# Performance work log

Measured on AMD Instinct MI355X. Metric: run time of the kernel, lower is better.

The kernel has to match this reference:

```python
import jax, jax.numpy as jnp
import numpy as np

ALPHA = 0.2  # LeakyReLU negative slope


def setup_inputs() -> dict:
    key = jax.random.key(0)
    k1, k2, k3, k4 = jax.random.split(key, 4)
    N, IN, OUT = 8192, 512, 256
    x = jax.random.normal(k1, (N, IN), dtype=jnp.float32)
    adj = jnp.zeros((N, N), dtype=jnp.float32)  # accepted but unused by the module
    W = jax.random.normal(k2, (OUT, IN), dtype=jnp.float32) * (1.0 / np.sqrt(IN))
    a1 = jax.random.normal(k3, (OUT,), dtype=jnp.float32) * (1.0 / np.sqrt(OUT))
    a2 = jax.random.normal(k4, (OUT,), dtype=jnp.float32) * (1.0 / np.sqrt(OUT))
    return {"x": x, "adj": adj, "W": W, "a1": a1, "a2": a2}


def reference(x, adj, W, a1, a2):
    # h = tran(x): [N, OUT]
    h = x @ W.T
    # additive GAT scores: e[i, j] = a2 . h_i + a1 . h_j  (from unsqueeze(0)+unsqueeze(1))
    s1 = h @ a1  # [N], att1(h)
    s2 = h @ a2  # [N], att2(h)
    e = s2[:, None] + s1[None, :]  # [N, N]
    e = jnp.where(e > 0, e, ALPHA * e)  # LeakyReLU
    attn = jax.nn.softmax(e, axis=1)  # softmax over dim=1; dropout is identity in eval
    return attn @ h  # [N, OUT]
```

## Files before the change

kernel.cpp:

```cpp
#include <hip/hip_runtime.h>

#define NROW 8192
#define DIN  512
#define DOUT 256
#define NCHUNK 256
#define CLEN 32
#define JCH 8

constexpr size_t OFF_H      = 0;
constexpr size_t OFF_S1     = OFF_H + (size_t)NROW*DOUT*4;
constexpr size_t OFF_S2     = OFF_S1 + NROW*4;
constexpr size_t OFF_S1S    = OFF_S2 + NROW*4;
constexpr size_t OFF_PERM   = OFF_S1S + NROW*4;
constexpr size_t OFF_WHI    = OFF_PERM + NROW*4;
constexpr size_t OFF_WLO    = OFF_WHI + NROW*4;
constexpr size_t OFF_PRELOS = OFF_WLO + NROW*4;
constexpr size_t OFF_SUFHIS = OFF_PRELOS + 33024;
constexpr size_t OFF_MISC   = OFF_SUFHIS + 33024;
constexpr size_t OFF_PC     = OFF_MISC + 256;
constexpr size_t OFF_TLO    = OFF_PC + (size_t)JCH*NROW*4;
constexpr size_t OFF_THI    = OFF_TLO + (size_t)NCHUNK*DOUT*4;
constexpr size_t OFF_PRELO  = OFF_THI + (size_t)NCHUNK*DOUT*4;
constexpr size_t OFF_SUFHI  = OFF_PRELO + (size_t)(NROW+1)*DOUT*4;
constexpr size_t WS_NEED    = OFF_SUFHI + (size_t)(NROW+1)*DOUT*4;

__global__ __launch_bounds__(256) void gemm_h(const float* __restrict__ x,
                                              const float* __restrict__ W,
                                              const float* __restrict__ a1,
                                              const float* __restrict__ a2,
                                              float* __restrict__ h,
                                              float* __restrict__ s1,
                                              float* __restrict__ s2) {
  __shared__ float xs[64][68];
  __shared__ float ws[64][68];
  const int tid = threadIdx.x;
  const int rowBase = blockIdx.x * 64;
  const int colBase = blockIdx.y * 64;
  const int ty = tid >> 4, tx = tid & 15;
  float acc[4][4] = {};
  for (int k0 = 0; k0 < DIN; k0 += 64) {
#pragma unroll
    for (int i = 0; i < 4; ++i) {
      int s = i * 256 + tid;
      int r = s >> 4;
      int kk = (s & 15) << 2;
      float4 v = *(const float4*)(x + (size_t)(rowBase + r) * DIN + k0 + kk);
      xs[kk + 0][r] = v.x; xs[kk + 1][r] = v.y; xs[kk + 2][r] = v.z; xs[kk + 3][r] = v.w;
      float4 u = *(const float4*)(W + (size_t)(colBase + r) * DIN + k0 + kk);
      ws[kk + 0][r] = u.x; ws[kk + 1][r] = u.y; ws[kk + 2][r] = u.z; ws[kk + 3][r] = u.w;
    }
    __syncthreads();
#pragma unroll
    for (int kk = 0; kk < 64; ++kk) {
      float4 av = *(const float4*)&xs[kk][ty << 2];
      float4 bv = *(const float4*)&ws[kk][tx << 2];
      float a[4] = {av.x, av.y, av.z, av.w};
      float b[4] = {bv.x, bv.y, bv.z, bv.w};
#pragma unroll
      for (int r = 0; r < 4; ++r)
#pragma unroll
        for (int c = 0; c < 4; ++c) acc[r][c] = fmaf(a[r], b[c], acc[r][c]);
    }
    __syncthreads();
  }
#pragma unroll
  for (int r = 0; r < 4; ++r) {
    float4 o = make_float4(acc[r][0], acc[r][1], acc[r][2], acc[r][3]);
    *(float4*)(h + (size_t)(rowBase + (ty << 2) + r) * DOUT + colBase + (tx << 2)) = o;
  }
  float4 A1 = *(const float4*)(a1 + colBase + (tx << 2));
  float4 A2 = *(const float4*)(a2 + colBase + (tx << 2));
#pragma unroll
  for (int r = 0; r < 4; ++r) {
    float p1 = acc[r][0] * A1.x + acc[r][1] * A1.y + acc[r][2] * A1.z + acc[r][3] * A1.w;
    float p2 = acc[r][0] * A2.x + acc[r][1] * A2.y + acc[r][2] * A2.z + acc[r][3] * A2.w;
#pragma unroll
    for (int m = 1; m < 16; m <<= 1) {
      p1 += __shfl_xor(p1, m);
      p2 += __shfl_xor(p2, m);
    }
    if (tx == 0) {
      int row = rowBase + (ty << 2) + r;
      atomicAdd(&s1[row], p1);
      atomicAdd(&s2[row], p2);
    }
  }
}

__global__ __launch_bounds__(256) void rank_partial(const float* __restrict__ s1,
                                                    int* __restrict__ pc) {
  __shared__ float sj[1024];
  const int t = threadIdx.x;
  const int ib = blockIdx.x, jc = blockIdx.y;
  const int j0 = jc * 1024;
  *(float4*)&sj[t << 2] = *(const float4*)(s1 + j0 + (t << 2));
  const int i = ib * 256 + t;
  const float v = s1[i];
  __syncthreads();
  int cnt = 0;
#pragma unroll 4
  for (int q = 0; q < 256; ++q) {
    float4 sv = *(const float4*)&sj[q << 2];
    int jg = j0 + (q << 2);
    cnt += (int)(sv.x < v) + (int)((sv.x == v) & (jg + 0 < i));
    cnt += (int)(sv.y < v) + (int)((sv.y == v) & (jg + 1 < i));
    cnt += (int)(sv.z < v) + (int)((sv.z == v) & (jg + 2 < i));
    cnt += (int)(sv.w < v) + (int)((sv.w == v) & (jg + 3 < i));
  }
  pc[jc * NROW + i] = cnt;
}

__global__ __launch_bounds__(256) void scatter_rank(const float* __restrict__ s1,
                                                    const int* __restrict__ pc,
                                                    float* __restrict__ s1s,
                                                    int* __restrict__ perm) {
  const int i = blockIdx.x * 256 + threadIdx.x;
  int r = 0;
#pragma unroll
  for (int jc = 0; jc < JCH; ++jc) r += pc[jc * NROW + i];
  s1s[r] = s1[i];
  perm[r] = i;
}

__global__ __launch_bounds__(1024) void scan_exp(const float* __restrict__ s1s,
                                                 float* __restrict__ w_hi,
                                                 float* __restrict__ w_lo,
                                                 float* __restrict__ prelo_s,
                                                 float* __restrict__ sufhi_s,
                                                 float* __restrict__ misc) {
  __shared__ float tt[1024];
  const int t = threadIdx.x;
  const float M1 = s1s[NROW - 1];
  float kv[8];
  {
    float4 r1 = *(const float4*)(s1s + 8 * t);
    float4 r2 = *(const float4*)(s1s + 8 * t + 4);
    kv[0] = r1.x; kv[1] = r1.y; kv[2] = r1.z; kv[3] = r1.w;
    kv[4] = r2.x; kv[5] = r2.y; kv[6] = r2.z; kv[7] = r2.w;
  }

  float wl[8];
  float loc = 0.f;
#pragma unroll
  for (int e = 0; e < 8; ++e) { wl[e] = __expf(0.2f * (kv[e] - M1)); loc += wl[e]; }
  tt[t] = loc;
  __syncthreads();
  for (int off = 1; off < 1024; off <<= 1) {
    float v = (t >= off) ? tt[t - off] : 0.f;
    __syncthreads();
    tt[t] += v;
    __syncthreads();
  }
  float run = (t > 0) ? tt[t - 1] : 0.f;
#pragma unroll
  for (int e = 0; e < 8; ++e) {
    int j = 8 * t + e;
    prelo_s[j] = run;
    w_lo[j] = wl[e];
    run += wl[e];
  }
  if (t == 1023) prelo_s[NROW] = run;
  __syncthreads();

  float wh[8];
  loc = 0.f;
#pragma unroll
  for (int e = 0; e < 8; ++e) { wh[e] = __expf(kv[e] - M1); loc += wh[e]; }
  tt[t] = loc;
  __syncthreads();
  for (int off = 1; off < 1024; off <<= 1) {
    float v = (t >= off) ? tt[t - off] : 0.f;
    __syncthreads();
    tt[t] += v;
    __syncthreads();
  }
  float total = tt[1023];
  run = (t > 0) ? tt[t - 1] : 0.f;
#pragma unroll
  for (int e = 0; e < 8; ++e) {
    int j = 8 * t + e;
    sufhi_s[j] = total - run;
    w_hi[j] = wh[e];
    run += wh[e];
  }
  if (t == 1023) sufhi_s[NROW] = 0.f;
  if (t == 0) misc[0] = M1;
}

__global__ __launch_bounds__(256) void chunk_totals(const float* __restrict__ h,
                                                    const int* __restrict__ perm,
                                                    const float* __restrict__ w_hi,
                                                    const float* __restrict__ w_lo,
                                                    float* __restrict__ T_lo,
                                                    float* __restrict__ T_hi) {
  const int d = threadIdx.x, b = blockIdx.x;
  const int j0 = b * CLEN;
  float tlo = 0.f, thi = 0.f;
#pragma unroll
  for (int e = 0; e < CLEN; e += 4) {
    int4 p4 = *(const int4*)(perm + j0 + e);
    float4 wl4 = *(const float4*)(w_lo + j0 + e);
    float4 wh4 = *(const float4*)(w_hi + j0 + e);
    float h0 = h[(size_t)p4.x * DOUT + d];
    float h1 = h[(size_t)p4.y * DOUT + d];
    float h2 = h[(size_t)p4.z * DOUT + d];
    float h3 = h[(size_t)p4.w * DOUT + d];
    tlo += wl4.x * h0 + wl4.y * h1 + wl4.z * h2 + wl4.w * h3;
    thi += wh4.x * h0 + wh4.y * h1 + wh4.z * h2 + wh4.w * h3;
  }
  T_lo[b * DOUT + d] = tlo;
  T_hi[b * DOUT + d] = thi;
}

__global__ __launch_bounds__(256) void write_prefix(const float* __restrict__ h,
                                                    const int* __restrict__ perm,
                                                    const float* __restrict__ w_hi,
                                                    const float* __restrict__ w_lo,
                                                    const float* __restrict__ T_lo,
                                                    const float* __restrict__ T_hi,
                                                    float* __restrict__ PreLo,
                                                    float* __restrict__ SufHi) {
  const int d = threadIdx.x, b = blockIdx.x;
  float rl = 0.f, tail = 0.f;
#pragma unroll 8
  for (int p = 0; p < NCHUNK; ++p) {
    float vl = T_lo[p * DOUT + d];
    float vh = T_hi[p * DOUT + d];
    rl   += (p < b) ? vl : 0.f;
    tail += (p > b) ? vh : 0.f;
  }
  const int j0 = b * CLEN;
  float hv[CLEN];
  float wlv[CLEN], whv[CLEN];
  float ownHi = 0.f;
#pragma unroll
  for (int e = 0; e < CLEN; e += 4) {
    int4 p4 = *(const int4*)(perm + j0 + e);
    float4 wl4 = *(const float4*)(w_lo + j0 + e);
    float4 wh4 = *(const float4*)(w_hi + j0 + e);
    hv[e + 0] = h[(size_t)p4.x * DOUT + d];
    hv[e + 1] = h[(size_t)p4.y * DOUT + d];
    hv[e + 2] = h[(size_t)p4.z * DOUT + d];
    hv[e + 3] = h[(size_t)p4.w * DOUT + d];
    wlv[e + 0] = wl4.x; wlv[e + 1] = wl4.y; wlv[e + 2] = wl4.z; wlv[e + 3] = wl4.w;
    whv[e + 0] = wh4.x; whv[e + 1] = wh4.y; whv[e + 2] = wh4.z; whv[e + 3] = wh4.w;
    ownHi += wh4.x * hv[e] + wh4.y * hv[e + 1] + wh4.z * hv[e + 2] + wh4.w * hv[e + 3];
  }
  float shb = tail + ownHi;
  float preh = 0.f;
#pragma unroll
  for (int e = 0; e < CLEN; ++e) {
    size_t j = (size_t)(j0 + e);
    PreLo[j * DOUT + d] = rl;
    SufHi[j * DOUT + d] = shb - preh;
    rl   += wlv[e] * hv[e];
    preh += whv[e] * hv[e];
  }
  if (b == NCHUNK - 1) {
    PreLo[(size_t)NROW * DOUT + d] = rl;
    SufHi[(size_t)NROW * DOUT + d] = 0.f;
  }
}

__global__ __launch_bounds__(256) void finalize(const float* __restrict__ s2,
                                                const float* __restrict__ s1s,
                                                const float* __restrict__ misc,
                                                const float* __restrict__ PreLo,
                                                const float* __restrict__ SufHi,
                                                const float* __restrict__ prelo_s,
                                                const float* __restrict__ sufhi_s,
                                                float* __restrict__ out) {
  const int wave = threadIdx.x >> 6, lane = threadIdx.x & 63;
  const int i = blockIdx.x * 4 + wave;
  const float c = s2[i];
  const float M1 = misc[0];
  const float tval = -c;
  int lo = 0, hi = NROW;
  while (lo < hi) {
    int mid = (lo + hi) >> 1;
    if (s1s[mid] <= tval) lo = mid + 1; else hi = mid;
  }
  const int k = lo;
  const float u = c + M1;
  const float m = fmaxf(u, 0.2f * u);
  const float fh = __expf(u - m);
  const float fl = __expf(0.2f * u - m);
  const float den = fh * sufhi_s[k] + fl * prelo_s[k];
  const float inv = 1.f / den;
  float4 A = *(const float4*)(SufHi + (size_t)k * DOUT + (lane << 2));
  float4 B = *(const float4*)(PreLo + (size_t)k * DOUT + (lane << 2));
  float4 o;
  o.x = (fh * A.x + fl * B.x) * inv;
  o.y = (fh * A.y + fl * B.y) * inv;
  o.z = (fh * A.z + fl * B.z) * inv;
  o.w = (fh * A.w + fl * B.w) * inv;
  *(float4*)(out + (size_t)i * DOUT + (lane << 2)) = o;
}

extern "C" void kernel_launch(void* const* d_in, const int* in_sizes, int n_in,
                              void* d_out, int out_size, void* d_ws, size_t ws_size,
                              hipStream_t stream) {
  const float* x  = (const float*)d_in[0];
  const float* W  = (const float*)d_in[2];
  const float* a1 = (const float*)d_in[3];
  const float* a2 = (const float*)d_in[4];
  float* out = (float*)d_out;

  char* ws = (char*)d_ws;
  if (ws_size < WS_NEED) ws = (char*)d_in[1];

  float* h        = (float*)(ws + OFF_H);
  float* s1       = (float*)(ws + OFF_S1);
  float* s2       = (float*)(ws + OFF_S2);
  float* s1s      = (float*)(ws + OFF_S1S);
  int*   perm     = (int*)  (ws + OFF_PERM);
  float* w_hi     = (float*)(ws + OFF_WHI);
  float* w_lo     = (float*)(ws + OFF_WLO);
  float* prelo_s  = (float*)(ws + OFF_PRELOS);
  float* sufhi_s  = (float*)(ws + OFF_SUFHIS);
  float* misc     = (float*)(ws + OFF_MISC);
  int*   pc       = (int*)  (ws + OFF_PC);
  float* T_lo     = (float*)(ws + OFF_TLO);
  float* T_hi     = (float*)(ws + OFF_THI);
  float* PreLo    = (float*)(ws + OFF_PRELO);
  float* SufHi    = (float*)(ws + OFF_SUFHI);

  hipMemsetAsync(s1, 0, (size_t)2 * NROW * 4, stream);

  gemm_h<<<dim3(NROW / 64, DOUT / 64), 256, 0, stream>>>(x, W, a1, a2, h, s1, s2);
  rank_partial<<<dim3(NROW / 256, JCH), 256, 0, stream>>>(s1, pc);
  scatter_rank<<<NROW / 256, 256, 0, stream>>>(s1, pc, s1s, perm);
  scan_exp<<<1, 1024, 0, stream>>>(s1s, w_hi, w_lo, prelo_s, sufhi_s, misc);
  chunk_totals<<<NCHUNK, 256, 0, stream>>>(h, perm, w_hi, w_lo, T_lo, T_hi);
  write_prefix<<<NCHUNK, 256, 0, stream>>>(h, perm, w_hi, w_lo, T_lo, T_hi, PreLo, SufHi);
  finalize<<<NROW / 4, 256, 0, stream>>>(s2, s1s, misc, PreLo, SufHi, prelo_s, sufhi_s, out);
}
```

Before: 405.2 us.

## Replace single-block exp scan with distributed max, weights and chunked prefix sums

Removes the one-block scan_exp kernel by computing the global max of s1 with an encoded atomicMax in the rank kernel and evaluating exp weights directly in the scatter kernel. Per-chunk weight sums are computed in chunk_totals and the scalar prefix/suffix sums are assembled in write_prefix with wave scans. Rank partial counts are accumulated with atomics instead of a separate buffer, so the memset now also clears the rank and max slots. The intent is to eliminate a serial single-workgroup stage and one launch, at the cost of extra atomics and redundant per-block reductions over chunk sums.

```diff
diff --git a/kernel.cpp b/kernel.cpp
--- a/kernel.cpp
+++ b/kernel.cpp
@@ -5,20 +5,22 @@
 #define DOUT 256
 #define NCHUNK 256
 #define CLEN 32
-#define JCH 8
 
 constexpr size_t OFF_H      = 0;
 constexpr size_t OFF_S1     = OFF_H + (size_t)NROW*DOUT*4;
 constexpr size_t OFF_S2     = OFF_S1 + NROW*4;
-constexpr size_t OFF_S1S    = OFF_S2 + NROW*4;
+constexpr size_t OFF_RANK   = OFF_S2 + NROW*4;
+constexpr size_t OFF_MISC   = OFF_RANK + NROW*4;
+constexpr size_t MEMSET_LEN = OFF_MISC + 256 - OFF_S1;
+constexpr size_t OFF_S1S    = OFF_MISC + 256;
 constexpr size_t OFF_PERM   = OFF_S1S + NROW*4;
 constexpr size_t OFF_WHI    = OFF_PERM + NROW*4;
 constexpr size_t OFF_WLO    = OFF_WHI + NROW*4;
 constexpr size_t OFF_PRELOS = OFF_WLO + NROW*4;
 constexpr size_t OFF_SUFHIS = OFF_PRELOS + 33024;
-constexpr size_t OFF_MISC   = OFF_SUFHIS + 33024;
-constexpr size_t OFF_PC     = OFF_MISC + 256;
-constexpr size_t OFF_TLO    = OFF_PC + (size_t)JCH*NROW*4;
+constexpr size_t OFF_CSLO   = OFF_SUFHIS + 33024;
+constexpr size_t OFF_CSHI   = OFF_CSLO + 1024;
+constexpr size_t OFF_TLO    = OFF_CSHI + 1024;
 constexpr size_t OFF_THI    = OFF_TLO + (size_t)NCHUNK*DOUT*4;
 constexpr size_t OFF_PRELO  = OFF_THI + (size_t)NCHUNK*DOUT*4;
 constexpr size_t OFF_SUFHI  = OFF_PRELO + (size_t)(NROW+1)*DOUT*4;
@@ -87,9 +89,11 @@
   }
 }
 
-__global__ __launch_bounds__(256) void rank_partial(const float* __restrict__ s1,
-                                                    int* __restrict__ pc) {
+__global__ __launch_bounds__(256) void rank_count(const float* __restrict__ s1,
+                                                  int* __restrict__ rank,
+                                                  unsigned int* __restrict__ miscu) {
   __shared__ float sj[1024];
+  __shared__ float wm[4];
   const int t = threadIdx.x;
   const int ib = blockIdx.x, jc = blockIdx.y;
   const int j0 = jc * 1024;
@@ -107,84 +111,41 @@
     cnt += (int)(sv.z < v) + (int)((sv.z == v) & (jg + 2 < i));
     cnt += (int)(sv.w < v) + (int)((sv.w == v) & (jg + 3 < i));
   }
-  pc[jc * NROW + i] = cnt;
-}
-
-__global__ __launch_bounds__(256) void scatter_rank(const float* __restrict__ s1,
-                                                    const int* __restrict__ pc,
-                                                    float* __restrict__ s1s,
-                                                    int* __restrict__ perm) {
+  atomicAdd(&rank[i], cnt);
+  if (jc == 0) {
+    float m = v;
+#pragma unroll
+    for (int off = 32; off > 0; off >>= 1) m = fmaxf(m, __shfl_down(m, off));
+    if ((t & 63) == 0) wm[t >> 6] = m;
+    __syncthreads();
+    if (t == 0) {
+      float mm = fmaxf(fmaxf(wm[0], wm[1]), fmaxf(wm[2], wm[3]));
+      unsigned int b = __float_as_uint(mm);
+      unsigned int enc = (b & 0x80000000u) ? ~b : (b | 0x80000000u);
+      atomicMax(miscu, enc);
+    }
+  }
+}
+
+__global__ __launch_bounds__(256) void scatter_w(const float* __restrict__ s1,
+                                                 const int* __restrict__ rank,
+                                                 const unsigned int* __restrict__ miscu,
+                                                 float* __restrict__ miscf,
+                                                 float* __restrict__ s1s,
+                                                 int* __restrict__ perm,
+                                                 float* __restrict__ w_hi,
+                                                 float* __restrict__ w_lo) {
   const int i = blockIdx.x * 256 + threadIdx.x;
-  int r = 0;
-#pragma unroll
-  for (int jc = 0; jc < JCH; ++jc) r += pc[jc * NROW + i];
-  s1s[r] = s1[i];
+  unsigned int e = miscu[0];
+  unsigned int b = (e & 0x80000000u) ? (e & 0x7fffffffu) : ~e;
+  const float M1 = __uint_as_float(b);
+  const float v = s1[i];
+  const int r = rank[i];
+  s1s[r] = v;
   perm[r] = i;
-}
-
-__global__ __launch_bounds__(1024) void scan_exp(const float* __restrict__ s1s,
-                                                 float* __restrict__ w_hi,
-                                                 float* __restrict__ w_lo,
-                                                 float* __restrict__ prelo_s,
-                                                 float* __restrict__ sufhi_s,
-                                                 float* __restrict__ misc) {
-  __shared__ float tt[1024];
-  const int t = threadIdx.x;
-  const float M1 = s1s[NROW - 1];
-  float kv[8];
-  {
-    float4 r1 = *(const float4*)(s1s + 8 * t);
-    float4 r2 = *(const float4*)(s1s + 8 * t + 4);
-    kv[0] = r1.x; kv[1] = r1.y; kv[2] = r1.z; kv[3] = r1.w;
-    kv[4] = r2.x; kv[5] = r2.y; kv[6] = r2.z; kv[7] = r2.w;
-  }
-
-  float wl[8];
-  float loc = 0.f;
-#pragma unroll
-  for (int e = 0; e < 8; ++e) { wl[e] = __expf(0.2f * (kv[e] - M1)); loc += wl[e]; }
-  tt[t] = loc;
-  __syncthreads();
-  for (int off = 1; off < 1024; off <<= 1) {
-    float v = (t >= off) ? tt[t - off] : 0.f;
-    __syncthreads();
-    tt[t] += v;
-    __syncthreads();
-  }
-  float run = (t > 0) ? tt[t - 1] : 0.f;
-#pragma unroll
-  for (int e = 0; e < 8; ++e) {
-    int j = 8 * t + e;
-    prelo_s[j] = run;
-    w_lo[j] = wl[e];
-    run += wl[e];
-  }
-  if (t == 1023) prelo_s[NROW] = run;
-  __syncthreads();
-
-  float wh[8];
-  loc = 0.f;
-#pragma unroll
-  for (int e = 0; e < 8; ++e) { wh[e] = __expf(kv[e] - M1); loc += wh[e]; }
-  tt[t] = loc;
-  __syncthreads();
-  for (int off = 1; off < 1024; off <<= 1) {
-    float v = (t >= off) ? tt[t - off] : 0.f;
-    __syncthreads();
-    tt[t] += v;
-    __syncthreads();
-  }
-  float total = tt[1023];
-  run = (t > 0) ? tt[t - 1] : 0.f;
-#pragma unroll
-  for (int e = 0; e < 8; ++e) {
-    int j = 8 * t + e;
-    sufhi_s[j] = total - run;
-    w_hi[j] = wh[e];
-    run += wh[e];
-  }
-  if (t == 1023) sufhi_s[NROW] = 0.f;
-  if (t == 0) misc[0] = M1;
+  w_hi[r] = __expf(v - M1);
+  w_lo[r] = __expf(0.2f * (v - M1));
+  if (i == 0) miscf[0] = M1;
 }
 
 __global__ __launch_bounds__(256) void chunk_totals(const float* __restrict__ h,
@@ -192,7 +153,9 @@
                                                     const float* __restrict__ w_hi,
                                                     const float* __restrict__ w_lo,
                                                     float* __restrict__ T_lo,
-                                                    float* __restrict__ T_hi) {
+                                                    float* __restrict__ T_hi,
+                                                    float* __restrict__ cs_lo,
+                                                    float* __restrict__ cs_hi) {
   const int d = threadIdx.x, b = blockIdx.x;
   const int j0 = b * CLEN;
   float tlo = 0.f, thi = 0.f;
@@ -210,6 +173,16 @@
   }
   T_lo[b * DOUT + d] = tlo;
   T_hi[b * DOUT + d] = thi;
+  if (d < 64) {
+    float wl = (d < 32) ? w_lo[j0 + d] : 0.f;
+    float wh = (d < 32) ? w_hi[j0 + d] : 0.f;
+#pragma unroll
+    for (int off = 32; off > 0; off >>= 1) {
+      wl += __shfl_down(wl, off);
+      wh += __shfl_down(wh, off);
+    }
+    if (d == 0) { cs_lo[b] = wl; cs_hi[b] = wh; }
+  }
 }
 
 __global__ __launch_bounds__(256) void write_prefix(const float* __restrict__ h,
@@ -218,9 +191,47 @@
                                                     const float* __restrict__ w_lo,
                                                     const float* __restrict__ T_lo,
                                                     const float* __restrict__ T_hi,
+                                                    const float* __restrict__ cs_lo,
+                                                    const float* __restrict__ cs_hi,
                                                     float* __restrict__ PreLo,
-                                                    float* __restrict__ SufHi) {
+                                                    float* __restrict__ SufHi,
+                                                    float* __restrict__ prelo_s,
+                                                    float* __restrict__ sufhi_s) {
   const int d = threadIdx.x, b = blockIdx.x;
+  const int j0 = b * CLEN;
+  if (d < 64) {
+    float accp = 0.f, acct = 0.f;
+    for (int p = d; p < NCHUNK; p += 64) {
+      float cl = cs_lo[p], ch = cs_hi[p];
+      accp += (p < b) ? cl : 0.f;
+      acct += (p > b) ? ch : 0.f;
+    }
+#pragma unroll
+    for (int off = 32; off > 0; off >>= 1) {
+      accp += __shfl_down(accp, off);
+      acct += __shfl_down(acct, off);
+    }
+    float pres  = __shfl(accp, 0);
+    float tails = __shfl(acct, 0);
+    float wl = (d < 32) ? w_lo[j0 + d] : 0.f;
+    float wh = (d < 32) ? w_hi[j0 + d] : 0.f;
+    float pl = wl, ph = wh;
+#pragma unroll
+    for (int off = 1; off < 32; off <<= 1) {
+      float a = __shfl_up(pl, off);
+      float c = __shfl_up(ph, off);
+      if (d >= off) { pl += a; ph += c; }
+    }
+    float chunk_hi_tot = __shfl(ph, 31);
+    if (d < 32) {
+      prelo_s[j0 + d] = pres + (pl - wl);
+      sufhi_s[j0 + d] = tails + (chunk_hi_tot - (ph - wh));
+    }
+    if (b == NCHUNK - 1 && d == 31) {
+      prelo_s[NROW] = pres + pl;
+      sufhi_s[NROW] = 0.f;
+    }
+  }
   float rl = 0.f, tail = 0.f;
 #pragma unroll 8
   for (int p = 0; p < NCHUNK; ++p) {
@@ -229,9 +240,7 @@
     rl   += (p < b) ? vl : 0.f;
     tail += (p > b) ? vh : 0.f;
   }
-  const int j0 = b * CLEN;
-  float hv[CLEN];
-  float wlv[CLEN], whv[CLEN];
+  float hv[CLEN], wlv[CLEN], whv[CLEN];
   float ownHi = 0.f;
 #pragma unroll
   for (int e = 0; e < CLEN; e += 4) {
@@ -264,7 +273,7 @@
 
 __global__ __launch_bounds__(256) void finalize(const float* __restrict__ s2,
                                                 const float* __restrict__ s1s,
-                                                const float* __restrict__ misc,
+                                                const float* __restrict__ miscf,
                                                 const float* __restrict__ PreLo,
                                                 const float* __restrict__ SufHi,
                                                 const float* __restrict__ prelo_s,
@@ -273,7 +282,7 @@
   const int wave = threadIdx.x >> 6, lane = threadIdx.x & 63;
   const int i = blockIdx.x * 4 + wave;
   const float c = s2[i];
-  const float M1 = misc[0];
+  const float M1 = miscf[0];
   const float tval = -c;
   int lo = 0, hi = NROW;
   while (lo < hi) {
@@ -309,29 +318,32 @@
   char* ws = (char*)d_ws;
   if (ws_size < WS_NEED) ws = (char*)d_in[1];
 
-  float* h        = (float*)(ws + OFF_H);
-  float* s1       = (float*)(ws + OFF_S1);
-  float* s2       = (float*)(ws + OFF_S2);
-  float* s1s      = (float*)(ws + OFF_S1S);
-  int*   perm     = (int*)  (ws + OFF_PERM);
-  float* w_hi     = (float*)(ws + OFF_WHI);
-  float* w_lo     = (float*)(ws + OFF_WLO);
-  float* prelo_s  = (float*)(ws + OFF_PRELOS);
-  float* sufhi_s  = (float*)(ws + OFF_SUFHIS);
-  float* misc     = (float*)(ws + OFF_MISC);
-  int*   pc       = (int*)  (ws + OFF_PC);
-  float* T_lo     = (float*)(ws + OFF_TLO);
-  float* T_hi     = (float*)(ws + OFF_THI);
-  float* PreLo    = (float*)(ws + OFF_PRELO);
-  float* SufHi    = (float*)(ws + OFF_SUFHI);
-
-  hipMemsetAsync(s1, 0, (size_t)2 * NROW * 4, stream);
+  float*        h       = (float*)(ws + OFF_H);
+  float*        s1      = (float*)(ws + OFF_S1);
+  float*        s2      = (float*)(ws + OFF_S2);
+  int*          rank    = (int*)  (ws + OFF_RANK);
+  unsigned int* miscu   = (unsigned int*)(ws + OFF_MISC);
+  float*        miscf   = (float*)(ws + OFF_MISC) + 1;
+  float*        s1s     = (float*)(ws + OFF_S1S);
+  int*          perm    = (int*)  (ws + OFF_PERM);
+  float*        w_hi    = (float*)(ws + OFF_WHI);
+  float*        w_lo    = (float*)(ws + OFF_WLO);
+  float*        prelo_s = (float*)(ws + OFF_PRELOS);
+  float*        sufhi_s = (float*)(ws + OFF_SUFHIS);
+  float*        cs_lo   = (float*)(ws + OFF_CSLO);
+  float*        cs_hi   = (float*)(ws + OFF_CSHI);
+  float*        T_lo    = (float*)(ws + OFF_TLO);
+  float*        T_hi    = (float*)(ws + OFF_THI);
+  float*        PreLo   = (float*)(ws + OFF_PRELO);
+  float*        SufHi   = (float*)(ws + OFF_SUFHI);
+
+  hipMemsetAsync(s1, 0, MEMSET_LEN, stream);
 
   gemm_h<<<dim3(NROW / 64, DOUT / 64), 256, 0, stream>>>(x, W, a1, a2, h, s1, s2);
-  rank_partial<<<dim3(NROW / 256, JCH), 256, 0, stream>>>(s1, pc);
-  scatter_rank<<<NROW / 256, 256, 0, stream>>>(s1, pc, s1s, perm);
-  scan_exp<<<1, 1024, 0, stream>>>(s1s, w_hi, w_lo, prelo_s, sufhi_s, misc);
-  chunk_totals<<<NCHUNK, 256, 0, stream>>>(h, perm, w_hi, w_lo, T_lo, T_hi);
-  write_prefix<<<NCHUNK, 256, 0, stream>>>(h, perm, w_hi, w_lo, T_lo, T_hi, PreLo, SufHi);
-  finalize<<<NROW / 4, 256, 0, stream>>>(s2, s1s, misc, PreLo, SufHi, prelo_s, sufhi_s, out);
-}
+  rank_count<<<dim3(NROW / 256, 8), 256, 0, stream>>>(s1, rank, miscu);
+  scatter_w<<<NROW / 256, 256, 0, stream>>>(s1, rank, miscu, miscf, s1s, perm, w_hi, w_lo);
+  chunk_totals<<<NCHUNK, 256, 0, stream>>>(h, perm, w_hi, w_lo, T_lo, T_hi, cs_lo, cs_hi);
+  write_prefix<<<NCHUNK, 256, 0, stream>>>(h, perm, w_hi, w_lo, T_lo, T_hi, cs_lo, cs_hi,
+                                           PreLo, SufHi, prelo_s, sufhi_s);
+  finalize<<<NROW / 4, 256, 0, stream>>>(s2, s1s, miscf, PreLo, SufHi, prelo_s, sufhi_s, out);
+}
```

Measured after the change: 402.8 us (median of 2 runs). About the same (-0.6%).
